# Performance work log

Measured on AMD Instinct MI355X. Metric: run time of the kernel, lower is better.

The kernel has to match this reference:

```python
import jax, jax.numpy as jnp
import numpy as np

H = 1024          # hid_dim
SEQ = 149         # input tokens (cls makes 150)
B = 128           # batch
WIN = 20          # local attention band half-width (hard-coded in module)


def _pe_table(n, d):
    # ConstantPE with period=1: position = 2*pi*arange(n)
    pos = 2.0 * np.pi * np.arange(n, dtype=np.float64)[:, None]
    div = np.exp(np.arange(0, d, 2, dtype=np.float64) * (-np.log(10000.0) / d))
    pe = np.zeros((n, d), dtype=np.float32)
    pe[:, 0::2] = np.sin(pos * div)
    pe[:, 1::2] = np.cos(pos * div)
    return jnp.asarray(pe)


def _band_mask(n, w=WIN):
    # True where attention is DISALLOWED (matches src_mask == 1)
    r = np.arange(n)[:, None]
    c = np.arange(n)[None, :]
    allowed = (c >= np.maximum(r - w, 0)) & (c < r + w)
    allowed[0, :] = True  # cls row attends everywhere
    return jnp.asarray(~allowed)


def _layer_norm(x, g, b, eps=1e-5):
    m = jnp.mean(x, axis=-1, keepdims=True)
    v = jnp.var(x, axis=-1, keepdims=True)
    return (x - m) * jax.lax.rsqrt(v + eps) * g + b


def setup_inputs() -> dict:
    key = jax.random.key(0)
    ks = jax.random.split(key, 8)
    s = 0.02
    return {
        "z": jax.random.normal(ks[0], (SEQ, B, H), jnp.float32),
        "cls_token": jax.random.normal(ks[1], (1, H), jnp.float32),
        "ln_g": jnp.ones((H,), jnp.float32),
        "ln_b": jnp.zeros((H,), jnp.float32),
        "w_qkv": jax.random.normal(ks[2], (H, 3 * H), jnp.float32) * s,
        "b_qkv": jnp.zeros((3 * H,), jnp.float32),
        "w_o": jax.random.normal(ks[3], (H, H), jnp.float32) * s,
        "b_o": jnp.zeros((H,), jnp.float32),
        "w_m1": jax.random.normal(ks[4], (H, H), jnp.float32) * s,
        "b_m1": jnp.zeros((H,), jnp.float32),
        "w_m2": jax.random.normal(ks[5], (H, H), jnp.float32) * s,
        "b_m2": jnp.zeros((H,), jnp.float32),
    }


def reference(z, cls_token, ln_g, ln_b, w_qkv, b_qkv, w_o, b_o, w_m1, b_m1, w_m2, b_m2):
    S1 = z.shape[0] + 1  # tokens incl. cls
    pe = _pe_table(S1, H)          # (S1, H)
    neg_mask = _band_mask(S1)      # (S1, S1) bool, True = masked

    x = jnp.swapaxes(z, 0, 1)                                   # (B, S, H)
    cls = jnp.broadcast_to(cls_token[None], (x.shape[0], 1, H))  # (B, 1, H)
    x = jnp.concatenate([cls, x], axis=1)                        # (B, S1, H)
    x = _layer_norm(x + pe[None], ln_g, ln_b)

    qkv = x @ w_qkv + b_qkv
    q, k, v = jnp.split(qkv, 3, axis=-1)

    attn = jnp.einsum("bqh,bkh->bqk", q, k) / jnp.sqrt(jnp.float32(H))
    attn = jnp.where(neg_mask[None], jnp.float32(-1e10), attn)
    attn = jax.nn.softmax(attn, axis=-1)

    sa = jnp.einsum("bqk,bkh->bqh", attn, v) @ w_o + b_o
    zsa = _layer_norm(x + sa, ln_g, ln_b)

    mlp = jax.nn.gelu(zsa @ w_m1 + b_m1, approximate=False) @ w_m2 + b_m2
    out = zsa + mlp
    return jnp.swapaxes(out, 0, 1)  # (S1, B, H)
```

## Files before the change

kernel.cpp:

```cpp
#include <hip/hip_runtime.h>
#include <math.h>

#define HD 1024
#define S1 150
#define BATCH 128
#define MTOK (S1 * BATCH)
#define WIN 20
#define QKVLD (3 * HD)

typedef unsigned short bf16_t;
typedef short s16x8 __attribute__((ext_vector_type(8)));
typedef float f32x4 __attribute__((ext_vector_type(4)));

__device__ __forceinline__ float bf2f(unsigned int u16) {
  return __uint_as_float(u16 << 16);
}
__device__ __forceinline__ unsigned short f2bf(float f) {
  unsigned int u = __float_as_uint(f);
  u += 0x7fff + ((u >> 16) & 1);
  return (unsigned short)(u >> 16);
}

__device__ __forceinline__ float wave_sum(float v) {
#pragma unroll
  for (int o = 32; o; o >>= 1) v += __shfl_down(v, o, 64);
  return v;
}
__device__ __forceinline__ float wave_max(float v) {
#pragma unroll
  for (int o = 32; o; o >>= 1) v = fmaxf(v, __shfl_down(v, o, 64));
  return v;
}

__device__ __forceinline__ void gload_lds16(const bf16_t* g, bf16_t* l) {
  __builtin_amdgcn_global_load_lds(
      (const __attribute__((address_space(1))) unsigned int*)(unsigned long long)(const void*)g,
      (__attribute__((address_space(3))) unsigned int*)(unsigned int)(unsigned long long)(void*)l,
      16, 0, 0);
}

__global__ __launch_bounds__(256) void transpose_kernel(
    const float* __restrict__ W, bf16_t* __restrict__ WT, int K, int N) {
  __shared__ float t[32][33];
  int n0 = blockIdx.x * 32, k0 = blockIdx.y * 32;
  int tx = threadIdx.x, ty = threadIdx.y;
#pragma unroll
  for (int i = 0; i < 4; i++)
    t[ty + i * 8][tx] = W[(size_t)(k0 + ty + i * 8) * N + n0 + tx];
  __syncthreads();
#pragma unroll
  for (int i = 0; i < 4; i++)
    WT[(size_t)(n0 + ty + i * 8) * K + k0 + tx] = f2bf(t[tx][ty + i * 8]);
}

__global__ void pe_kernel(float* __restrict__ pe) {
  int s = blockIdx.x;
  double pos = 6.283185307179586476925286766559 * (double)s;
  for (int p = threadIdx.x; p < HD / 2; p += blockDim.x) {
    double dv = exp((double)(2 * p) * (-9.210340371976184 / (double)HD));
    double a = pos * dv;
    pe[s * HD + 2 * p] = (float)sin(a);
    pe[s * HD + 2 * p + 1] = (float)cos(a);
  }
}

__global__ __launch_bounds__(256) void build_x_kernel(
    const float* __restrict__ z, const float* __restrict__ cls,
    const float* __restrict__ pe, const float* __restrict__ g,
    const float* __restrict__ be, bf16_t* __restrict__ x) {
  int t = blockIdx.x;
  int b = t / S1, s = t % S1;
  const float* src = (s == 0) ? cls : (z + ((size_t)(s - 1) * BATCH + b) * HD);
  const float* pr = pe + (size_t)s * HD;
  int tid = threadIdx.x;
  float vals[4];
  float sum = 0.f, sq = 0.f;
#pragma unroll
  for (int i = 0; i < 4; i++) {
    int h = tid + i * 256;
    float v = src[h] + pr[h];
    vals[i] = v;
    sum += v;
    sq += v * v;
  }
  __shared__ float shs[4], shq[4];
  __shared__ float sm, sr;
  sum = wave_sum(sum);
  sq = wave_sum(sq);
  int wave = tid >> 6, lane = tid & 63;
  if (!lane) { shs[wave] = sum; shq[wave] = sq; }
  __syncthreads();
  if (!tid) {
    float S = shs[0] + shs[1] + shs[2] + shs[3];
    float Q = shq[0] + shq[1] + shq[2] + shq[3];
    float mean = S * (1.f / HD);
    float var = Q * (1.f / HD) - mean * mean;
    sm = mean;
    sr = rsqrtf(var + 1e-5f);
  }
  __syncthreads();
  float mean = sm, rstd = sr;
  bf16_t* xr = x + (size_t)t * HD;
#pragma unroll
  for (int i = 0; i < 4; i++) {
    int h = tid + i * 256;
    xr[h] = f2bf((vals[i] - mean) * rstd * g[h] + be[h]);
  }
}

__global__ __launch_bounds__(256) void ln_residual_kernel(
    const bf16_t* __restrict__ a, const bf16_t* __restrict__ r,
    const float* __restrict__ g, const float* __restrict__ be,
    bf16_t* __restrict__ out) {
  int t = blockIdx.x;
  int tid = threadIdx.x;
  const bf16_t* ar = a + (size_t)t * QKVLD;
  const bf16_t* rr = r + (size_t)t * HD;
  float vals[4];
  float sum = 0.f, sq = 0.f;
#pragma unroll
  for (int i = 0; i < 4; i++) {
    int h = tid + i * 256;
    float v = bf2f(ar[h]) + bf2f(rr[h]);
    vals[i] = v;
    sum += v;
    sq += v * v;
  }
  __shared__ float shs[4], shq[4];
  __shared__ float sm, sr;
  sum = wave_sum(sum);
  sq = wave_sum(sq);
  int wave = tid >> 6, lane = tid & 63;
  if (!lane) { shs[wave] = sum; shq[wave] = sq; }
  __syncthreads();
  if (!tid) {
    float S = shs[0] + shs[1] + shs[2] + shs[3];
    float Q = shq[0] + shq[1] + shq[2] + shq[3];
    float mean = S * (1.f / HD);
    float var = Q * (1.f / HD) - mean * mean;
    sm = mean;
    sr = rsqrtf(var + 1e-5f);
  }
  __syncthreads();
  float mean = sm, rstd = sr;
  bf16_t* outp = out + (size_t)t * QKVLD;
#pragma unroll
  for (int i = 0; i < 4; i++) {
    int h = tid + i * 256;
    outp[h] = f2bf((vals[i] - mean) * rstd * g[h] + be[h]);
  }
}

template <int EPI>
__global__ __launch_bounds__(256) void mfma_gemm_kernel(
    const bf16_t* __restrict__ A, int lda, const bf16_t* __restrict__ WT,
    const float* __restrict__ bias, bf16_t* __restrict__ C, int ldc, int N) {
  constexpr int K = 1024;
  __shared__ bf16_t As[128 * 32];
  __shared__ bf16_t Bs[128 * 32];
  int tid = threadIdx.x;
  int w = tid >> 6, lane = tid & 63;
  int wm = w >> 1, wn = w & 1;
  int m0 = blockIdx.y * 128, n0 = blockIdx.x * 128;

  int srow = lane >> 2;
  int scol = ((lane & 3) ^ ((lane >> 3) & 3)) * 8;
  const bf16_t* gA0 = A + (size_t)(m0 + w * 32 + srow) * lda + scol;
  const bf16_t* gA1 = gA0 + (size_t)16 * lda;
  const bf16_t* gB0 = WT + (size_t)(n0 + w * 32 + srow) * K + scol;
  const bf16_t* gB1 = gB0 + (size_t)16 * K;
  bf16_t* lA0 = As + (w * 32) * 32;
  bf16_t* lA1 = As + (w * 32 + 16) * 32;
  bf16_t* lB0 = Bs + (w * 32) * 32;
  bf16_t* lB1 = Bs + (w * 32 + 16) * 32;

  int frow = lane & 15;
  int slot = (lane >> 4) ^ ((frow >> 1) & 3);
  int aoff[4], boff[4];
#pragma unroll
  for (int t = 0; t < 4; t++) {
    aoff[t] = (wm * 64 + t * 16 + frow) * 32 + slot * 8;
    boff[t] = (wn * 64 + t * 16 + frow) * 32 + slot * 8;
  }

  f32x4 acc[4][4] = {};

  for (int k0 = 0; k0 < K; k0 += 32) {
    gload_lds16(gA0, lA0);
    gload_lds16(gA1, lA1);
    gload_lds16(gB0, lB0);
    gload_lds16(gB1, lB1);
    gA0 += 32; gA1 += 32; gB0 += 32; gB1 += 32;
    __syncthreads();
    s16x8 af[4], bf[4];
#pragma unroll
    for (int t = 0; t < 4; t++) {
      af[t] = *(const s16x8*)(As + aoff[t]);
      bf[t] = *(const s16x8*)(Bs + boff[t]);
    }
#pragma unroll
    for (int i = 0; i < 4; i++)
#pragma unroll
      for (int j = 0; j < 4; j++)
        acc[i][j] = __builtin_amdgcn_mfma_f32_16x16x32_bf16(af[i], bf[j], acc[i][j], 0, 0, 0);
    __syncthreads();
  }

  int erow = (lane >> 4) * 4, ecol = lane & 15;
#pragma unroll
  for (int j = 0; j < 4; j++) {
    int n = n0 + wn * 64 + j * 16 + ecol;
    float bb = bias[n];
#pragma unroll
    for (int i = 0; i < 4; i++) {
      int mb = m0 + wm * 64 + i * 16 + erow;
#pragma unroll
      for (int r = 0; r < 4; r++) {
        float v = acc[i][j][r] + bb;
        if (EPI == 1) v = 0.5f * v * (1.f + erff(v * 0.7071067811865476f));
        C[(size_t)(mb + r) * ldc + n] = f2bf(v);
      }
    }
  }
}

__global__ __launch_bounds__(256) void mfma_gemm_out_kernel(
    const bf16_t* __restrict__ A, int lda, const bf16_t* __restrict__ WT,
    const float* __restrict__ bias, const bf16_t* __restrict__ res,
    float* __restrict__ out) {
  constexpr int K = 1024;
  __shared__ bf16_t As[128 * 32];
  __shared__ bf16_t Bs[128 * 32];
  int tid = threadIdx.x;
  int w = tid >> 6, lane = tid & 63;
  int wm = w >> 1, wn = w & 1;
  int m0 = blockIdx.y * 128, n0 = blockIdx.x * 128;

  int srow = lane >> 2;
  int scol = ((lane & 3) ^ ((lane >> 3) & 3)) * 8;
  const bf16_t* gA0 = A + (size_t)(m0 + w * 32 + srow) * lda + scol;
  const bf16_t* gA1 = gA0 + (size_t)16 * lda;
  const bf16_t* gB0 = WT + (size_t)(n0 + w * 32 + srow) * K + scol;
  const bf16_t* gB1 = gB0 + (size_t)16 * K;
  bf16_t* lA0 = As + (w * 32) * 32;
  bf16_t* lA1 = As + (w * 32 + 16) * 32;
  bf16_t* lB0 = Bs + (w * 32) * 32;
  bf16_t* lB1 = Bs + (w * 32 + 16) * 32;

  int frow = lane & 15;
  int slot = (lane >> 4) ^ ((frow >> 1) & 3);
  int aoff[4], boff[4];
#pragma unroll
  for (int t = 0; t < 4; t++) {
    aoff[t] = (wm * 64 + t * 16 + frow) * 32 + slot * 8;
    boff[t] = (wn * 64 + t * 16 + frow) * 32 + slot * 8;
  }

  f32x4 acc[4][4] = {};

  for (int k0 = 0; k0 < K; k0 += 32) {
    gload_lds16(gA0, lA0);
    gload_lds16(gA1, lA1);
    gload_lds16(gB0, lB0);
    gload_lds16(gB1, lB1);
    gA0 += 32; gA1 += 32; gB0 += 32; gB1 += 32;
    __syncthreads();
    s16x8 af[4], bf[4];
#pragma unroll
    for (int t = 0; t < 4; t++) {
      af[t] = *(const s16x8*)(As + aoff[t]);
      bf[t] = *(const s16x8*)(Bs + boff[t]);
    }
#pragma unroll
    for (int i = 0; i < 4; i++)
#pragma unroll
      for (int j = 0; j < 4; j++)
        acc[i][j] = __builtin_amdgcn_mfma_f32_16x16x32_bf16(af[i], bf[j], acc[i][j], 0, 0, 0);
    __syncthreads();
  }

  int erow = (lane >> 4) * 4, ecol = lane & 15;
#pragma unroll
  for (int j = 0; j < 4; j++) {
    int n = n0 + wn * 64 + j * 16 + ecol;
    float bb = bias[n];
#pragma unroll
    for (int i = 0; i < 4; i++) {
      int mb = m0 + wm * 64 + i * 16 + erow;
#pragma unroll
      for (int r = 0; r < 4; r++) {
        int m = mb + r;
        int b = m / S1, s = m % S1;
        float v = acc[i][j][r] + bb + bf2f(res[(size_t)m * QKVLD + n]);
        out[((size_t)s * BATCH + b) * HD + n] = v;
      }
    }
  }
}

__global__ __launch_bounds__(256) void attn_kernel(bf16_t* __restrict__ qkv) {
  int lin = blockIdx.x;
  int tok = ((lin & 7) * (MTOK / 8)) + (lin >> 3);
  int b = tok / S1, qi = tok % S1;
  bf16_t* qp = qkv + (size_t)tok * QKVLD;
  const bf16_t* kbase = qkv + (size_t)b * S1 * QKVLD + HD;
  const bf16_t* vbase = qkv + (size_t)b * S1 * QKVLD + 2 * HD;
  __shared__ float probs[S1];
  __shared__ float rb1[4], rb2[4];
  int tid = threadIdx.x;
  int wave = tid >> 6, lane = tid & 63;
  int lo = (qi == 0) ? 0 : (qi - WIN > 0 ? qi - WIN : 0);
  int hi = (qi == 0) ? S1 : (qi + WIN < S1 ? qi + WIN : S1);

  float qf[16];
  {
    uint4 a = *(const uint4*)(qp + lane * 16);
    uint4 c4 = *(const uint4*)(qp + lane * 16 + 8);
    unsigned int u[8] = {a.x, a.y, a.z, a.w, c4.x, c4.y, c4.z, c4.w};
#pragma unroll
    for (int i = 0; i < 8; i++) {
      qf[2 * i] = bf2f(u[i] & 0xffffu);
      qf[2 * i + 1] = bf2f(u[i] >> 16);
    }
  }

  for (int c = lo + wave; c < hi; c += 4) {
    const bf16_t* kr = kbase + (size_t)c * QKVLD + lane * 16;
    uint4 a = *(const uint4*)kr;
    uint4 c4 = *(const uint4*)(kr + 8);
    unsigned int u[8] = {a.x, a.y, a.z, a.w, c4.x, c4.y, c4.z, c4.w};
    float s = 0.f;
#pragma unroll
    for (int i = 0; i < 8; i++) {
      s += qf[2 * i] * bf2f(u[i] & 0xffffu);
      s += qf[2 * i + 1] * bf2f(u[i] >> 16);
    }
    s = wave_sum(s);
    if (!lane) probs[c] = s * 0.03125f;
  }
  __syncthreads();

  float lm = -1e30f;
  for (int c = lo + tid; c < hi; c += 256) lm = fmaxf(lm, probs[c]);
  lm = wave_max(lm);
  if (!lane) rb1[wave] = lm;
  __syncthreads();
  float bmax = fmaxf(fmaxf(rb1[0], rb1[1]), fmaxf(rb1[2], rb1[3]));
  float ls = 0.f;
  for (int c = lo + tid; c < hi; c += 256) {
    float e = expf(probs[c] - bmax);
    probs[c] = e;
    ls += e;
  }
  ls = wave_sum(ls);
  if (!lane) rb2[wave] = ls;
  __syncthreads();
  float inv = 1.f / (rb2[0] + rb2[1] + rb2[2] + rb2[3]);
  for (int c = lo + tid; c < hi; c += 256) probs[c] *= inv;
  __syncthreads();

  float a0 = 0.f, a1 = 0.f, a2 = 0.f, a3 = 0.f;
  const bf16_t* vp = vbase + 4 * tid;
  for (int c = lo; c < hi; ++c) {
    float p = probs[c];
    uint2 vv = *(const uint2*)(vp + (size_t)c * QKVLD);
    a0 += p * bf2f(vv.x & 0xffffu);
    a1 += p * bf2f(vv.x >> 16);
    a2 += p * bf2f(vv.y & 0xffffu);
    a3 += p * bf2f(vv.y >> 16);
  }
  uint2 pk;
  pk.x = (unsigned int)f2bf(a0) | ((unsigned int)f2bf(a1) << 16);
  pk.y = (unsigned int)f2bf(a2) | ((unsigned int)f2bf(a3) << 16);
  *(uint2*)(qp + 4 * tid) = pk;
}

extern "C" void kernel_launch(void* const* d_in, const int* in_sizes, int n_in,
                              void* d_out, int out_size, void* d_ws, size_t ws_size,
                              hipStream_t stream) {
  (void)in_sizes; (void)n_in; (void)out_size; (void)ws_size;
  const float* z = (const float*)d_in[0];
  const float* cls = (const float*)d_in[1];
  const float* ln_g = (const float*)d_in[2];
  const float* ln_b = (const float*)d_in[3];
  const float* w_qkv = (const float*)d_in[4];
  const float* b_qkv = (const float*)d_in[5];
  const float* w_o = (const float*)d_in[6];
  const float* b_o = (const float*)d_in[7];
  const float* w_m1 = (const float*)d_in[8];
  const float* b_m1 = (const float*)d_in[9];
  const float* w_m2 = (const float*)d_in[10];
  const float* b_m2 = (const float*)d_in[11];

  char* wsb = (char*)d_ws;
  bf16_t* wt_m2 = (bf16_t*)wsb;
  float* pe = (float*)(wsb + 2097152);
  bf16_t* qkv = (bf16_t*)(wsb + 2097152 + 614400);

  char* outb = (char*)d_out;
  bf16_t* x = (bf16_t*)outb;
  bf16_t* wt_qkv = (bf16_t*)(outb + 39321600);
  bf16_t* wt_o = (bf16_t*)(outb + 45613056);
  bf16_t* wt_m1 = (bf16_t*)(outb + 47710208);

  bf16_t* av = qkv;
  bf16_t* sa = qkv + HD;
  bf16_t* zsa = qkv + 2 * HD;
  bf16_t* h1 = qkv;
  float* out = (float*)d_out;

  transpose_kernel<<<dim3(96, 32), dim3(32, 8), 0, stream>>>(w_qkv, wt_qkv, HD, 3 * HD);
  transpose_kernel<<<dim3(32, 32), dim3(32, 8), 0, stream>>>(w_o, wt_o, HD, HD);
  transpose_kernel<<<dim3(32, 32), dim3(32, 8), 0, stream>>>(w_m1, wt_m1, HD, HD);
  transpose_kernel<<<dim3(32, 32), dim3(32, 8), 0, stream>>>(w_m2, wt_m2, HD, HD);
  pe_kernel<<<S1, 256, 0, stream>>>(pe);
  build_x_kernel<<<MTOK, 256, 0, stream>>>(z, cls, pe, ln_g, ln_b, x);
  mfma_gemm_kernel<0><<<dim3(24, 150), 256, 0, stream>>>(
      x, HD, wt_qkv, b_qkv, qkv, QKVLD, 3 * HD);
  attn_kernel<<<MTOK, 256, 0, stream>>>(qkv);
  mfma_gemm_kernel<0><<<dim3(8, 150), 256, 0, stream>>>(
      av, QKVLD, wt_o, b_o, sa, QKVLD, HD);
  ln_residual_kernel<<<MTOK, 256, 0, stream>>>(sa, x, ln_g, ln_b, zsa);
  mfma_gemm_kernel<1><<<dim3(8, 150), 256, 0, stream>>>(
      zsa, QKVLD, wt_m1, b_m1, h1, QKVLD, HD);
  mfma_gemm_out_kernel<<<dim3(8, 150), 256, 0, stream>>>(
      h1, QKVLD, wt_m2, b_m2, zsa, out);
}
```

Baseline: 742.6 us.

## Tile attention over 32-query blocks with MFMA scores and shared V reuse

Replaces the one-block-per-token attention kernel with one that handles 32 queries per block. Q·K scores for the band are computed with bf16 MFMA through LDS staging, and softmax runs over a shared score tile. Each wave then accumulates P·V for 8 queries at once, so V rows are reused across queries instead of re-read for every token. The cost is more LDS, masked wasted MFMA work outside the band, and heavy register use from the 64-float accumulator.

New measurement: 707.3 us. -4.8%, faster.

```diff
diff --git a/kernel.cpp b/kernel.cpp
--- a/kernel.cpp
+++ b/kernel.cpp
@@ -24,11 +24,6 @@
 __device__ __forceinline__ float wave_sum(float v) {
 #pragma unroll
   for (int o = 32; o; o >>= 1) v += __shfl_down(v, o, 64);
-  return v;
-}
-__device__ __forceinline__ float wave_max(float v) {
-#pragma unroll
-  for (int o = 32; o; o >>= 1) v = fmaxf(v, __shfl_down(v, o, 64));
   return v;
 }
 
@@ -298,81 +293,168 @@
   }
 }
 
-__global__ __launch_bounds__(256) void attn_kernel(bf16_t* __restrict__ qkv) {
-  int lin = blockIdx.x;
-  int tok = ((lin & 7) * (MTOK / 8)) + (lin >> 3);
-  int b = tok / S1, qi = tok % S1;
-  bf16_t* qp = qkv + (size_t)tok * QKVLD;
-  const bf16_t* kbase = qkv + (size_t)b * S1 * QKVLD + HD;
-  const bf16_t* vbase = qkv + (size_t)b * S1 * QKVLD + 2 * HD;
-  __shared__ float probs[S1];
-  __shared__ float rb1[4], rb2[4];
+__global__ __launch_bounds__(256) void attn_tile_kernel(bf16_t* __restrict__ qkv) {
+  int g = blockIdx.x;
+  int xcd = g & 7, tt0 = g >> 3;
+  int qt = tt0 % 5, b = xcd + 8 * (tt0 / 5);
+  int q0 = qt * 32;
+
+  int lo_col = (qt == 0) ? 0 : (q0 - 20);
+  int hi_col = (qt == 0) ? 150 : ((q0 + 51 < 150) ? q0 + 51 : 150);
+  int ct0 = lo_col >> 5;
+  int cth = (hi_col + 31) >> 5;
+  int NCT = cth - ct0;
+  int W = NCT * 32;
+  int NSUB = NCT * 2;
+  int NT = 2 * NSUB;
+  int T = NT >> 2;
+
+  __shared__ bf16_t Qs[2 * 32 * 32];
+  __shared__ bf16_t Ks[2 * 160 * 32];
+  __shared__ float S[32][164];
+
   int tid = threadIdx.x;
-  int wave = tid >> 6, lane = tid & 63;
-  int lo = (qi == 0) ? 0 : (qi - WIN > 0 ? qi - WIN : 0);
-  int hi = (qi == 0) ? S1 : (qi + WIN < S1 ? qi + WIN : S1);
-
-  float qf[16];
+  int w = tid >> 6, lane = tid & 63;
+
+  const bf16_t* kvbase = qkv + (size_t)b * S1 * QKVLD;
+
+  int sr = lane >> 2;
+  int scol = ((lane & 3) ^ ((lane >> 3) & 3)) * 8;
+  int frow = lane & 15;
+  int fslot = (((lane >> 4) ^ ((frow >> 1) & 3))) * 8;
+
+  f32x4 acc[5] = {};
+
+  int U1 = 2 + NSUB;
+
+  for (int k0 = 0; k0 < 1024; k0 += 64) {
+    for (int uu = w; uu < 2 * U1; uu += 4) {
+      int p = (uu >= U1) ? 1 : 0;
+      int ur = uu - p * U1;
+      int col = k0 + p * 32 + scol;
+      if (ur < 2) {
+        int qrow = q0 + ur * 16 + sr;
+        if (qrow > 149) qrow = 149;
+        gload_lds16(kvbase + (size_t)qrow * QKVLD + col,
+                    Qs + p * 1024 + (ur * 16) * 32);
+      } else {
+        int cr0 = (ur - 2) * 16;
+        int cg = ct0 * 32 + cr0 + sr;
+        if (cg > 149) cg = 149;
+        gload_lds16(kvbase + (size_t)cg * QKVLD + HD + col,
+                    Ks + p * 5120 + cr0 * 32);
+      }
+    }
+    __syncthreads();
+    s16x8 af0[2], af1[2];
+#pragma unroll
+    for (int p = 0; p < 2; p++) {
+      af0[p] = *(const s16x8*)(Qs + p * 1024 + (0 * 16 + frow) * 32 + fslot);
+      af1[p] = *(const s16x8*)(Qs + p * 1024 + (1 * 16 + frow) * 32 + fslot);
+    }
+#pragma unroll
+    for (int t = 0; t < 5; t++) {
+      if (t < T) {
+        int tidt = w + t * 4;
+        int qs = (tidt >= NSUB) ? 1 : 0;
+        int cs = tidt - qs * NSUB;
+#pragma unroll
+        for (int p = 0; p < 2; p++) {
+          s16x8 bf = *(const s16x8*)(Ks + p * 5120 + (cs * 16 + frow) * 32 + fslot);
+          s16x8 a = qs ? af1[p] : af0[p];
+          acc[t] = __builtin_amdgcn_mfma_f32_16x16x32_bf16(a, bf, acc[t], 0, 0, 0);
+        }
+      }
+    }
+    __syncthreads();
+  }
+
+  int erow = (lane >> 4) * 4, ecol = lane & 15;
+#pragma unroll
+  for (int t = 0; t < 5; t++) {
+    if (t < T) {
+      int tidt = w + t * 4;
+      int qs = (tidt >= NSUB) ? 1 : 0;
+      int cs = tidt - qs * NSUB;
+#pragma unroll
+      for (int r = 0; r < 4; r++) {
+        int qrel = qs * 16 + erow + r;
+        int crel = cs * 16 + ecol;
+        int qg = q0 + qrel, cg = ct0 * 32 + crel;
+        bool ok = (qg < 150) && (cg < 150) &&
+                  ((qg == 0) || (cg >= qg - WIN && cg < qg + WIN));
+        S[qrel][crel] = ok ? acc[t][r] * 0.03125f : -1e30f;
+      }
+    }
+  }
+  __syncthreads();
+
   {
-    uint4 a = *(const uint4*)(qp + lane * 16);
-    uint4 c4 = *(const uint4*)(qp + lane * 16 + 8);
-    unsigned int u[8] = {a.x, a.y, a.z, a.w, c4.x, c4.y, c4.z, c4.w};
-#pragma unroll
-    for (int i = 0; i < 8; i++) {
-      qf[2 * i] = bf2f(u[i] & 0xffffu);
-      qf[2 * i + 1] = bf2f(u[i] >> 16);
-    }
-  }
-
-  for (int c = lo + wave; c < hi; c += 4) {
-    const bf16_t* kr = kbase + (size_t)c * QKVLD + lane * 16;
-    uint4 a = *(const uint4*)kr;
-    uint4 c4 = *(const uint4*)(kr + 8);
-    unsigned int u[8] = {a.x, a.y, a.z, a.w, c4.x, c4.y, c4.z, c4.w};
+    int q = tid >> 3, j = tid & 7;
+    float m = -1e30f;
+    for (int c = j; c < W; c += 8) m = fmaxf(m, S[q][c]);
+#pragma unroll
+    for (int o = 1; o < 8; o <<= 1) m = fmaxf(m, __shfl_xor(m, o, 64));
     float s = 0.f;
-#pragma unroll
-    for (int i = 0; i < 8; i++) {
-      s += qf[2 * i] * bf2f(u[i] & 0xffffu);
-      s += qf[2 * i + 1] * bf2f(u[i] >> 16);
-    }
-    s = wave_sum(s);
-    if (!lane) probs[c] = s * 0.03125f;
-  }
-  __syncthreads();
-
-  float lm = -1e30f;
-  for (int c = lo + tid; c < hi; c += 256) lm = fmaxf(lm, probs[c]);
-  lm = wave_max(lm);
-  if (!lane) rb1[wave] = lm;
-  __syncthreads();
-  float bmax = fmaxf(fmaxf(rb1[0], rb1[1]), fmaxf(rb1[2], rb1[3]));
-  float ls = 0.f;
-  for (int c = lo + tid; c < hi; c += 256) {
-    float e = expf(probs[c] - bmax);
-    probs[c] = e;
-    ls += e;
-  }
-  ls = wave_sum(ls);
-  if (!lane) rb2[wave] = ls;
-  __syncthreads();
-  float inv = 1.f / (rb2[0] + rb2[1] + rb2[2] + rb2[3]);
-  for (int c = lo + tid; c < hi; c += 256) probs[c] *= inv;
-  __syncthreads();
-
-  float a0 = 0.f, a1 = 0.f, a2 = 0.f, a3 = 0.f;
-  const bf16_t* vp = vbase + 4 * tid;
-  for (int c = lo; c < hi; ++c) {
-    float p = probs[c];
-    uint2 vv = *(const uint2*)(vp + (size_t)c * QKVLD);
-    a0 += p * bf2f(vv.x & 0xffffu);
-    a1 += p * bf2f(vv.x >> 16);
-    a2 += p * bf2f(vv.y & 0xffffu);
-    a3 += p * bf2f(vv.y >> 16);
-  }
-  uint2 pk;
-  pk.x = (unsigned int)f2bf(a0) | ((unsigned int)f2bf(a1) << 16);
-  pk.y = (unsigned int)f2bf(a2) | ((unsigned int)f2bf(a3) << 16);
-  *(uint2*)(qp + 4 * tid) = pk;
+    for (int c = j; c < W; c += 8) {
+      float e = __expf(S[q][c] - m);
+      S[q][c] = e;
+      s += e;
+    }
+#pragma unroll
+    for (int o = 1; o < 8; o <<= 1) s += __shfl_xor(s, o, 64);
+    float inv = 1.f / s;
+    for (int c = j; c < W; c += 8) S[q][c] *= inv;
+  }
+  __syncthreads();
+
+  int qg0 = q0 + 8 * w;
+  if (qg0 < 150) {
+    int lo = (qt == 0 && w == 0) ? 0 : ((qg0 - WIN > 0) ? qg0 - WIN : 0);
+    int hi = (qt == 0 && w == 0) ? 150 : ((qg0 + 27 < 150) ? qg0 + 27 : 150);
+    int c0base = ct0 * 32;
+#pragma unroll
+    for (int hp = 0; hp < 2; hp++) {
+      int hb = hp * 512 + lane * 8;
+      float a[8][8];
+#pragma unroll
+      for (int qi = 0; qi < 8; qi++)
+#pragma unroll
+        for (int e = 0; e < 8; e++) a[qi][e] = 0.f;
+      const bf16_t* vb = kvbase + 2 * HD + hb;
+      for (int c = lo; c < hi; ++c) {
+        uint4 vv = *(const uint4*)(vb + (size_t)c * QKVLD);
+        float vf[8];
+        vf[0] = __uint_as_float(vv.x << 16);
+        vf[1] = __uint_as_float(vv.x & 0xffff0000u);
+        vf[2] = __uint_as_float(vv.y << 16);
+        vf[3] = __uint_as_float(vv.y & 0xffff0000u);
+        vf[4] = __uint_as_float(vv.z << 16);
+        vf[5] = __uint_as_float(vv.z & 0xffff0000u);
+        vf[6] = __uint_as_float(vv.w << 16);
+        vf[7] = __uint_as_float(vv.w & 0xffff0000u);
+        int crel = c - c0base;
+#pragma unroll
+        for (int qi = 0; qi < 8; qi++) {
+          float p = S[8 * w + qi][crel];
+#pragma unroll
+          for (int e = 0; e < 8; e++) a[qi][e] += p * vf[e];
+        }
+      }
+#pragma unroll
+      for (int qi = 0; qi < 8; qi++) {
+        int qg = qg0 + qi;
+        if (qg < 150) {
+          uint4 pk;
+          pk.x = (unsigned int)f2bf(a[qi][0]) | ((unsigned int)f2bf(a[qi][1]) << 16);
+          pk.y = (unsigned int)f2bf(a[qi][2]) | ((unsigned int)f2bf(a[qi][3]) << 16);
+          pk.z = (unsigned int)f2bf(a[qi][4]) | ((unsigned int)f2bf(a[qi][5]) << 16);
+          pk.w = (unsigned int)f2bf(a[qi][6]) | ((unsigned int)f2bf(a[qi][7]) << 16);
+          *(uint4*)(qkv + ((size_t)b * S1 + qg) * QKVLD + hb) = pk;
+        }
+      }
+    }
+  }
 }
 
 extern "C" void kernel_launch(void* const* d_in, const int* in_sizes, int n_in,
@@ -417,7 +499,7 @@
   build_x_kernel<<<MTOK, 256, 0, stream>>>(z, cls, pe, ln_g, ln_b, x);
   mfma_gemm_kernel<0><<<dim3(24, 150), 256, 0, stream>>>(
       x, HD, wt_qkv, b_qkv, qkv, QKVLD, 3 * HD);
-  attn_kernel<<<MTOK, 256, 0, stream>>>(qkv);
+  attn_tile_kernel<<<640, 256, 0, stream>>>(qkv);
   mfma_gemm_kernel<0><<<dim3(8, 150), 256, 0, stream>>>(
       av, QKVLD, wt_o, b_o, sa, QKVLD, HD);
   ln_residual_kernel<<<MTOK, 256, 0, stream>>>(sa, x, ln_g, ln_b, zsa);
```
